# Performance work log

Hardware: AMD Instinct MI355X
Metric: run time of the kernel (lower is better)

The kernel has to match this reference:

```python
import jax, jax.numpy as jnp
import numpy as np

N, E, G = 50000, 400000, 2000
H, HEADS, HD = 128, 4, 32


def setup_inputs() -> dict:
    key = jax.random.key(0)
    ks = jax.random.split(key, 16)
    nrm = lambda k, shape, s=0.05: jax.random.normal(k, shape, dtype=jnp.float32) * s
    inp = {}
    inp["x"] = jax.random.normal(ks[0], (N, 39), dtype=jnp.float32)
    inp["edge_index"] = jax.random.randint(ks[1], (2, E), 0, N, dtype=jnp.int32)
    inp["edge_attr"] = jax.random.normal(ks[2], (E, 8), dtype=jnp.float32)
    inp["batch"] = jnp.sort(jax.random.randint(ks[3], (N,), 0, G, dtype=jnp.int32))
    inp["in_W"] = nrm(ks[4], (39, H)); inp["in_b"] = jnp.zeros((H,), jnp.float32)
    inp["in_g"] = jnp.ones((H,), jnp.float32); inp["in_beta"] = jnp.zeros((H,), jnp.float32)
    inp["Wl"] = nrm(ks[5], (3, H, H)); inp["Wr"] = nrm(ks[6], (3, H, H))
    inp["We"] = nrm(ks[7], (3, 8, H)); inp["att"] = nrm(ks[8], (3, HEADS, HD))
    inp["conv_b"] = jnp.zeros((3, H), jnp.float32)
    inp["bn_g"] = jnp.ones((3, H), jnp.float32); inp["bn_b"] = jnp.zeros((3, H), jnp.float32)
    inp["t1_W"] = nrm(ks[9], (3 * H, 256)); inp["t1_b"] = jnp.zeros((256,), jnp.float32)
    inp["t1_g"] = jnp.ones((256,), jnp.float32); inp["t1_beta"] = jnp.zeros((256,), jnp.float32)
    inp["t2_W"] = nrm(ks[10], (256, 128)); inp["t2_b"] = jnp.zeros((128,), jnp.float32)
    inp["t2_g"] = jnp.ones((128,), jnp.float32); inp["t2_beta"] = jnp.zeros((128,), jnp.float32)
    inp["head_W"] = nrm(ks[11], (128, 12)); inp["head_b"] = jnp.zeros((12,), jnp.float32)
    return inp


def _bn(h, g, b):
    # BatchNorm1d in training mode: normalize with batch statistics.
    m = h.mean(0)
    v = ((h - m) ** 2).mean(0)
    return g * (h - m) * jax.lax.rsqrt(v + 1e-5) + b


def reference(x, edge_index, edge_attr, batch, in_W, in_b, in_g, in_beta,
              Wl, Wr, We, att, conv_b, bn_g, bn_b,
              t1_W, t1_b, t1_g, t1_beta, t2_W, t2_b, t2_g, t2_beta,
              head_W, head_b):
    src, dst = edge_index[0], edge_index[1]  # messages flow src -> dst (PyG convention)
    xn = jax.nn.relu(_bn(x @ in_W + in_b, in_g, in_beta))  # [N, H]
    for l in range(3):  # three residual GATv2 layers
        xl = (xn @ Wl[l]).reshape(N, HEADS, HD)  # lin_l (source transform)
        xr = (xn @ Wr[l]).reshape(N, HEADS, HD)  # lin_r (target transform)
        ep = (edge_attr @ We[l]).reshape(E, HEADS, HD)
        m = jax.nn.leaky_relu(xl[src] + xr[dst] + ep, 0.2)  # [E, HEADS, HD]
        alpha = jnp.einsum('ehd,hd->eh', m, att[l])  # [E, HEADS]
        amax = jax.ops.segment_max(alpha, dst, num_segments=N)
        amax = jnp.where(jnp.isfinite(amax), amax, 0.0)  # nodes with no in-edges
        ae = jnp.exp(alpha - amax[dst])
        denom = jax.ops.segment_sum(ae, dst, num_segments=N)
        a = ae / (denom[dst] + 1e-16)  # scatter-softmax over neighborhoods
        agg = jax.ops.segment_sum(xl[src] * a[:, :, None], dst, num_segments=N)
        h = agg.reshape(N, H) + conv_b[l]
        h = jax.nn.elu(_bn(h, bn_g[l], bn_b[l]))
        xn = xn + h
    # 3-way global pooling per graph
    cnt = jax.ops.segment_sum(jnp.ones((N,), jnp.float32), batch, num_segments=G)
    sadd = jax.ops.segment_sum(xn, batch, num_segments=G)
    smean = sadd / jnp.maximum(cnt, 1.0)[:, None]
    smax = jax.ops.segment_max(xn, batch, num_segments=G)
    smax = jnp.where(cnt[:, None] > 0, smax, 0.0)
    xg = jnp.concatenate([smean, smax, sadd], axis=1)  # [G, 3H]
    t = jax.nn.relu(_bn(xg @ t1_W + t1_b, t1_g, t1_beta))
    t = jax.nn.relu(_bn(t @ t2_W + t2_b, t2_g, t2_beta))
    return jax.nn.sigmoid(t @ head_W + head_b)  # [G, 12]
```

## Files before the change

kernel.cpp:

```cpp
#include <hip/hip_runtime.h>
#include <math.h>


constexpr int N_ = 50000;
constexpr int E_ = 400000;
constexpr int G_ = 2000;
constexpr int H_ = 128;
constexpr int IN_ = 39;

__global__ __launch_bounds__(256) void hist_kernel(const int* __restrict__ keys, int n,
                                                   int* __restrict__ cnt) {
  for (int i = blockIdx.x * 256 + threadIdx.x; i < n; i += gridDim.x * 256)
    atomicAdd(&cnt[keys[i]], 1);
}

__global__ __launch_bounds__(1024) void scan_excl4(const int* __restrict__ in,
                                                   int* __restrict__ out, int n) {
  __shared__ int wsum[16];
  __shared__ int carry_s, chunk_tot;
  int t = threadIdx.x, lane = t & 63, wid = t >> 6;
  if (t == 0) carry_s = 0;
  __syncthreads();
  for (int base = 0; base < n; base += 4096) {
    int idx = base + t * 4;
    int4 v = make_int4(0, 0, 0, 0);
    if (idx + 3 < n) {
      v = *(const int4*)&in[idx];
    } else {
      if (idx < n) v.x = in[idx];
      if (idx + 1 < n) v.y = in[idx + 1];
      if (idx + 2 < n) v.z = in[idx + 2];
      if (idx + 3 < n) v.w = in[idx + 3];
    }
    int tsum = v.x + v.y + v.z + v.w;
    int x = tsum;
#pragma unroll
    for (int off = 1; off < 64; off <<= 1) {
      int y = __shfl_up(x, off, 64);
      if (lane >= off) x += y;
    }
    if (lane == 63) wsum[wid] = x;
    __syncthreads();
    if (t == 0) {
      int acc = 0;
#pragma unroll
      for (int w = 0; w < 16; w++) { int tmp = wsum[w]; wsum[w] = acc; acc += tmp; }
      chunk_tot = acc;
    }
    __syncthreads();
    int base_ex = carry_s + wsum[wid] + x - tsum;
    if (idx < n) out[idx] = base_ex;
    if (idx + 1 < n) out[idx + 1] = base_ex + v.x;
    if (idx + 2 < n) out[idx + 2] = base_ex + v.x + v.y;
    if (idx + 3 < n) out[idx + 3] = base_ex + v.x + v.y + v.z;
    __syncthreads();
    if (t == 0) carry_s += chunk_tot;
    __syncthreads();
  }
  if (t == 0) out[n] = carry_s;
}

__global__ __launch_bounds__(256) void goff_from_sorted(const int* __restrict__ batch,
                                                        int* __restrict__ goff) {
  int i = blockIdx.x * 256 + threadIdx.x;
  if (i >= N_) return;
  int bi = batch[i];
  int bp = (i == 0) ? -1 : batch[i - 1];
  for (int g = bp + 1; g <= bi; g++) goff[g] = i;
  if (i == N_ - 1) {
    for (int g = bi + 1; g <= G_; g++) goff[g] = N_;
  }
}

__global__ __launch_bounds__(256) void edge_scatter(const int* __restrict__ ei,
                                                    const float* __restrict__ ea,
                                                    int* __restrict__ cursor,
                                                    int* __restrict__ esrc,
                                                    float* __restrict__ eas) {
  int e = blockIdx.x * 256 + threadIdx.x;
  if (e >= E_) return;
  int src = ei[e];
  int dst = ei[E_ + e];
  int j = atomicAdd(&cursor[dst], 1);
  esrc[j] = src;
  const float4* eav = (const float4*)(ea + (size_t)e * 8);
  float4* dstp = (float4*)(eas + (size_t)j * 8);
  dstp[0] = eav[0];
  dstp[1] = eav[1];
}

__global__ __launch_bounds__(256) void in_gemm(const float* __restrict__ x,
                                               const float* __restrict__ W,
                                               const float* __restrict__ b,
                                               float* __restrict__ y,
                                               float* __restrict__ ssum,
                                               float* __restrict__ ssq) {
  __shared__ float xs[32][40];
  __shared__ float s1[256], s2[256];
  int t = threadIdx.x;
  int row0 = blockIdx.x * 32;
  for (int i = t; i < 32 * IN_; i += 256) {
    int r = i / IN_, k = i % IN_;
    int row = row0 + r;
    xs[r][k] = (row < N_) ? x[row * IN_ + k] : 0.f;
  }
  __syncthreads();
  int col = t & 127;
  int half = t >> 7;
  float acc[16];
#pragma unroll
  for (int r = 0; r < 16; r++) acc[r] = 0.f;
  for (int k = 0; k < IN_; k++) {
    float w = W[k * H_ + col];
#pragma unroll
    for (int r = 0; r < 16; r++) acc[r] = fmaf(xs[half * 16 + r][k], w, acc[r]);
  }
  float bb = b[col];
  float a1 = 0.f, a2 = 0.f;
#pragma unroll
  for (int r = 0; r < 16; r++) {
    int row = row0 + half * 16 + r;
    float v = acc[r] + bb;
    if (row < N_) {
      y[row * H_ + col] = v;
      a1 += v;
      a2 = fmaf(v, v, a2);
    }
  }
  s1[t] = a1; s2[t] = a2;
  __syncthreads();
  if (t < 128) {
    atomicAdd(&ssum[t], s1[t] + s1[t + 128]);
    atomicAdd(&ssq[t], s2[t] + s2[t + 128]);
  }
}

__global__ __launch_bounds__(256) void gemm_xlxr(const float* __restrict__ xn,
                                                 const float* __restrict__ Wlp,
                                                 const float* __restrict__ Wrp,
                                                 float* __restrict__ xl,
                                                 float* __restrict__ xr) {
  __shared__ float xs[64][16];
  __shared__ float wl_s[16][128];
  __shared__ float wr_s[16][128];
  int t = threadIdx.x;
  int tx = t & 31;
  int ty = t >> 5;
  int row0 = blockIdx.x * 64;
  float4 accl[8], accr[8];
#pragma unroll
  for (int r = 0; r < 8; r++) {
    accl[r] = make_float4(0.f, 0.f, 0.f, 0.f);
    accr[r] = make_float4(0.f, 0.f, 0.f, 0.f);
  }
  for (int kc = 0; kc < H_; kc += 16) {
    __syncthreads();
    {
      int r = t >> 2;
      int k4 = (t & 3) * 4;
      int row = row0 + r;
      float4 v = (row < N_) ? *(const float4*)&xn[row * H_ + kc + k4]
                            : make_float4(0.f, 0.f, 0.f, 0.f);
      *(float4*)&xs[r][k4] = v;
    }
    for (int i = t; i < 512; i += 256) {
      int k = i >> 5;
      int c4 = (i & 31) * 4;
      *(float4*)&wl_s[k][c4] = *(const float4*)&Wlp[(kc + k) * H_ + c4];
      *(float4*)&wr_s[k][c4] = *(const float4*)&Wrp[(kc + k) * H_ + c4];
    }
    __syncthreads();
#pragma unroll
    for (int k = 0; k < 16; k += 4) {
      float4 xv[8];
#pragma unroll
      for (int r = 0; r < 8; r++) xv[r] = *(const float4*)&xs[ty * 8 + r][k];
#pragma unroll
      for (int kk = 0; kk < 4; kk++) {
        float4 wl = *(const float4*)&wl_s[k + kk][tx * 4];
        float4 wr = *(const float4*)&wr_s[k + kk][tx * 4];
#pragma unroll
        for (int r = 0; r < 8; r++) {
          float xvr = (kk == 0) ? xv[r].x : (kk == 1) ? xv[r].y : (kk == 2) ? xv[r].z : xv[r].w;
          accl[r].x = fmaf(xvr, wl.x, accl[r].x);
          accl[r].y = fmaf(xvr, wl.y, accl[r].y);
          accl[r].z = fmaf(xvr, wl.z, accl[r].z);
          accl[r].w = fmaf(xvr, wl.w, accl[r].w);
          accr[r].x = fmaf(xvr, wr.x, accr[r].x);
          accr[r].y = fmaf(xvr, wr.y, accr[r].y);
          accr[r].z = fmaf(xvr, wr.z, accr[r].z);
          accr[r].w = fmaf(xvr, wr.w, accr[r].w);
        }
      }
    }
  }
#pragma unroll
  for (int r = 0; r < 8; r++) {
    int row = row0 + ty * 8 + r;
    if (row < N_) {
      *(float4*)&xl[row * H_ + tx * 4] = accl[r];
      *(float4*)&xr[row * H_ + tx * 4] = accr[r];
    }
  }
}

__device__ __forceinline__ float epcalc(const float4& a0, const float4& a1, const float w[8]) {
  float ep = a0.x * w[0];
  ep = fmaf(a0.y, w[1], ep);
  ep = fmaf(a0.z, w[2], ep);
  ep = fmaf(a0.w, w[3], ep);
  ep = fmaf(a1.x, w[4], ep);
  ep = fmaf(a1.y, w[5], ep);
  ep = fmaf(a1.z, w[6], ep);
  ep = fmaf(a1.w, w[7], ep);
  return ep;
}

__global__ __launch_bounds__(256) void agg_csr(const int* __restrict__ eoff,
                                               const int* __restrict__ esrc,
                                               const float* __restrict__ eas,
                                               const float* __restrict__ Wel,
                                               const float* __restrict__ attl,
                                               const float* __restrict__ xl,
                                               const float* __restrict__ xr,
                                               const float* __restrict__ cb,
                                               float* __restrict__ buf,
                                               float* __restrict__ ssum,
                                               float* __restrict__ ssq) {
  __shared__ float s1[256], s2[256];
  int t = threadIdx.x;
  int lane = t & 127;
  int sub = t >> 7;
  float w[8];
#pragma unroll
  for (int k = 0; k < 8; k++) w[k] = Wel[k * H_ + lane];
  float attv = attl[lane];
  float cbv = cb[lane];
  float a1 = 0.f, a2 = 0.f;
  for (int n = blockIdx.x * 2 + sub; n < N_; n += gridDim.x * 2) {
    float xrv = xr[n * H_ + lane];
    int e0 = eoff[n], e1 = eoff[n + 1];
    float acc = 0.f, den = 0.f;
    int j = e0;
    for (; j + 4 <= e1; j += 4) {
      int s0 = esrc[j], s1i = esrc[j + 1], s2i = esrc[j + 2], s3 = esrc[j + 3];
      const float4* ep0 = (const float4*)(eas + (size_t)j * 8);
      float4 a00 = ep0[0], a01 = ep0[1];
      float4 a10 = ep0[2], a11 = ep0[3];
      float4 a20 = ep0[4], a21 = ep0[5];
      float4 a30 = ep0[6], a31 = ep0[7];
      float x0 = xl[s0 * H_ + lane];
      float x1 = xl[s1i * H_ + lane];
      float x2 = xl[s2i * H_ + lane];
      float x3 = xl[s3 * H_ + lane];
      float m0 = x0 + xrv + epcalc(a00, a01, w);
      float m1 = x1 + xrv + epcalc(a10, a11, w);
      float m2 = x2 + xrv + epcalc(a20, a21, w);
      float m3 = x3 + xrv + epcalc(a30, a31, w);
      m0 = (m0 > 0.f) ? m0 : 0.2f * m0;
      m1 = (m1 > 0.f) ? m1 : 0.2f * m1;
      m2 = (m2 > 0.f) ? m2 : 0.2f * m2;
      m3 = (m3 > 0.f) ? m3 : 0.2f * m3;
      float p0 = m0 * attv, p1 = m1 * attv, p2 = m2 * attv, p3 = m3 * attv;
#pragma unroll
      for (int off = 16; off > 0; off >>= 1) {
        p0 += __shfl_xor(p0, off, 64);
        p1 += __shfl_xor(p1, off, 64);
        p2 += __shfl_xor(p2, off, 64);
        p3 += __shfl_xor(p3, off, 64);
      }
      float e0v = __expf(p0), e1v = __expf(p1), e2v = __expf(p2), e3v = __expf(p3);
      acc = fmaf(e0v, x0, acc);
      acc = fmaf(e1v, x1, acc);
      acc = fmaf(e2v, x2, acc);
      acc = fmaf(e3v, x3, acc);
      den += (e0v + e1v) + (e2v + e3v);
    }
    for (; j < e1; j++) {
      int src = esrc[j];
      const float4* eap = (const float4*)(eas + (size_t)j * 8);
      float4 ea0 = eap[0], ea1 = eap[1];
      float xlv = xl[src * H_ + lane];
      float m = xlv + xrv + epcalc(ea0, ea1, w);
      m = (m > 0.f) ? m : 0.2f * m;
      float p = m * attv;
#pragma unroll
      for (int off = 16; off > 0; off >>= 1) p += __shfl_xor(p, off, 64);
      float ae = __expf(p);
      acc = fmaf(ae, xlv, acc);
      den += ae;
    }
    float h = acc / (den + 1e-16f) + cbv;
    buf[n * H_ + lane] = h;
    a1 += h;
    a2 = fmaf(h, h, a2);
  }
  s1[t] = a1; s2[t] = a2;
  __syncthreads();
  if (t < 128) {
    atomicAdd(&ssum[t], s1[t] + s1[t + 128]);
    atomicAdd(&ssq[t], s2[t] + s2[t + 128]);
  }
}

__global__ void bn_final(const float* __restrict__ ssum, const float* __restrict__ ssq,
                         float rows_inv, int cols, float* __restrict__ mean,
                         float* __restrict__ rstd) {
  int c = threadIdx.x;
  if (c < cols) {
    float m = ssum[c] * rows_inv;
    float v = ssq[c] * rows_inv - m * m;
    mean[c] = m;
    rstd[c] = rsqrtf(v + 1e-5f);
  }
}

__global__ __launch_bounds__(256) void apply_bn_relu(const float* __restrict__ y,
                                                     float* __restrict__ out,
                                                     const float* __restrict__ g,
                                                     const float* __restrict__ beta,
                                                     const float* __restrict__ mean,
                                                     const float* __restrict__ rstd,
                                                     long total, int cmask) {
  long i = (long)blockIdx.x * 256 + threadIdx.x;
  if (i >= total) return;
  int c = (int)i & cmask;
  float v = g[c] * (y[i] - mean[c]) * rstd[c] + beta[c];
  out[i] = fmaxf(v, 0.f);
}

__global__ __launch_bounds__(256) void node_residual(float* __restrict__ xn,
                                                     const float* __restrict__ buf,
                                                     const float* __restrict__ g,
                                                     const float* __restrict__ beta,
                                                     const float* __restrict__ mean,
                                                     const float* __restrict__ rstd) {
  int i = blockIdx.x * 256 + threadIdx.x;
  if (i >= N_ * H_) return;
  int c = i & 127;
  float v = g[c] * (buf[i] - mean[c]) * rstd[c] + beta[c];
  v = (v > 0.f) ? v : (__expf(v) - 1.f);
  xn[i] += v;
}

__global__ __launch_bounds__(128) void pool_csr(const int* __restrict__ goff,
                                                const float* __restrict__ xn,
                                                float* __restrict__ xg) {
  int g = blockIdx.x;
  int t = threadIdx.x;
  int n0 = goff[g], n1 = goff[g + 1];
  float s = 0.f, mx = -INFINITY;
  for (int n = n0; n < n1; n++) {
    float v = xn[n * H_ + t];
    s += v;
    mx = fmaxf(mx, v);
  }
  float c = (float)(n1 - n0);
  xg[g * 384 + t] = s / fmaxf(c, 1.f);
  xg[g * 384 + 128 + t] = (c > 0.f) ? mx : 0.f;
  xg[g * 384 + 256 + t] = s;
}

template <int K, int COLS>
__global__ void mlp_gemm(const float* __restrict__ A, const float* __restrict__ W,
                         const float* __restrict__ b, float* __restrict__ Y, int rows,
                         float* __restrict__ ssum, float* __restrict__ ssq) {
  __shared__ float xs[8][K];
  int t = threadIdx.x;
  int row0 = blockIdx.x * 8;
  for (int i = t; i < 8 * K; i += COLS) {
    int r = i / K, k = i % K;
    int row = row0 + r;
    xs[r][k] = (row < rows) ? A[row * K + k] : 0.f;
  }
  __syncthreads();
  float acc[8];
#pragma unroll
  for (int r = 0; r < 8; r++) acc[r] = 0.f;
  for (int k = 0; k < K; k++) {
    float w = W[k * COLS + t];
#pragma unroll
    for (int r = 0; r < 8; r++) acc[r] = fmaf(xs[r][k], w, acc[r]);
  }
  float bb = b[t];
  float a1 = 0.f, a2 = 0.f;
#pragma unroll
  for (int r = 0; r < 8; r++) {
    int row = row0 + r;
    if (row < rows) {
      float v = acc[r] + bb;
      Y[row * COLS + t] = v;
      a1 += v;
      a2 = fmaf(v, v, a2);
    }
  }
  atomicAdd(&ssum[t], a1);
  atomicAdd(&ssq[t], a2);
}

__global__ __launch_bounds__(64) void head_kernel(const float* __restrict__ u,
                                                  const float* __restrict__ W,
                                                  const float* __restrict__ b,
                                                  float* __restrict__ out) {
  __shared__ float row[128];
  int g = blockIdx.x;
  int t = threadIdx.x;
  row[t] = u[g * 128 + t];
  row[t + 64] = u[g * 128 + 64 + t];
  __syncthreads();
  if (t < 12) {
    float acc = b[t];
    for (int k = 0; k < 128; k++) acc = fmaf(row[k], W[k * 12 + t], acc);
    out[g * 12 + t] = 1.f / (1.f + expf(-acc));
  }
}

extern "C" void kernel_launch(void* const* d_in, const int* in_sizes, int n_in, void* d_out,
                              int out_size, void* d_ws, size_t ws_size, hipStream_t stream) {
  (void)in_sizes; (void)n_in; (void)out_size; (void)ws_size;
  const float* x       = (const float*)d_in[0];
  const int*   ei      = (const int*)d_in[1];
  const float* ea      = (const float*)d_in[2];
  const int*   batch   = (const int*)d_in[3];
  const float* in_W    = (const float*)d_in[4];
  const float* in_b    = (const float*)d_in[5];
  const float* in_g    = (const float*)d_in[6];
  const float* in_beta = (const float*)d_in[7];
  const float* Wl      = (const float*)d_in[8];
  const float* Wr      = (const float*)d_in[9];
  const float* We      = (const float*)d_in[10];
  const float* att     = (const float*)d_in[11];
  const float* conv_b  = (const float*)d_in[12];
  const float* bn_g    = (const float*)d_in[13];
  const float* bn_b    = (const float*)d_in[14];
  const float* t1_W    = (const float*)d_in[15];
  const float* t1_b    = (const float*)d_in[16];
  const float* t1_g    = (const float*)d_in[17];
  const float* t1_beta = (const float*)d_in[18];
  const float* t2_W    = (const float*)d_in[19];
  const float* t2_b    = (const float*)d_in[20];
  const float* t2_g    = (const float*)d_in[21];
  const float* t2_beta = (const float*)d_in[22];
  const float* head_W  = (const float*)d_in[23];
  const float* head_b  = (const float*)d_in[24];
  float* out = (float*)d_out;

  float* p = (float*)d_ws;
  float* xn   = p; p += N_ * H_;
  float* xl   = p; p += N_ * H_;
  float* xr   = p; p += N_ * H_;
  float* buf  = p; p += N_ * H_;
  float* ssum = p; p += 256;
  float* ssq  = p; p += 256;
  float* mean = p; p += 256;
  float* rstd = p; p += 256;
  float* xg   = p; p += G_ * 384;
  float* u1   = p; p += G_ * 256;
  float* u2   = p; p += G_ * 128;
  float* eas  = p; p += (size_t)E_ * 8;
  int* ip = (int*)p;
  int* deg    = ip; ip += N_;
  int* eoff   = ip; ip += N_ + 1;
  int* cursor = ip; ip += N_;
  int* goff   = ip; ip += G_ + 1;
  int* esrc   = ip; ip += E_;

  const int EW_GRID = 25000;

  hipMemsetAsync(deg, 0, (size_t)N_ * sizeof(int), stream);
  hist_kernel<<<1024, 256, 0, stream>>>(ei + E_, E_, deg);
  scan_excl4<<<1, 1024, 0, stream>>>(deg, eoff, N_);
  hipMemcpyAsync(cursor, eoff, (size_t)N_ * sizeof(int), hipMemcpyDeviceToDevice, stream);
  edge_scatter<<<(E_ + 255) / 256, 256, 0, stream>>>(ei, ea, cursor, esrc, eas);
  goff_from_sorted<<<(N_ + 255) / 256, 256, 0, stream>>>(batch, goff);

  hipMemsetAsync(ssum, 0, 512 * sizeof(float), stream);
  in_gemm<<<(N_ + 31) / 32, 256, 0, stream>>>(x, in_W, in_b, buf, ssum, ssq);
  bn_final<<<1, 256, 0, stream>>>(ssum, ssq, 1.f / N_, H_, mean, rstd);
  apply_bn_relu<<<EW_GRID, 256, 0, stream>>>(buf, xn, in_g, in_beta, mean, rstd,
                                             (long)N_ * H_, 127);

  for (int l = 0; l < 3; l++) {
    gemm_xlxr<<<(N_ + 63) / 64, 256, 0, stream>>>(xn, Wl + l * H_ * H_, Wr + l * H_ * H_, xl, xr);
    hipMemsetAsync(ssum, 0, 512 * sizeof(float), stream);
    agg_csr<<<4096, 256, 0, stream>>>(eoff, esrc, eas, We + l * 8 * H_, att + l * H_,
                                      xl, xr, conv_b + l * H_, buf, ssum, ssq);
    bn_final<<<1, 256, 0, stream>>>(ssum, ssq, 1.f / N_, H_, mean, rstd);
    node_residual<<<EW_GRID, 256, 0, stream>>>(xn, buf, bn_g + l * H_, bn_b + l * H_, mean, rstd);
  }

  pool_csr<<<G_, 128, 0, stream>>>(goff, xn, xg);

  hipMemsetAsync(ssum, 0, 512 * sizeof(float), stream);
  mlp_gemm<384, 256><<<G_ / 8, 256, 0, stream>>>(xg, t1_W, t1_b, u1, G_, ssum, ssq);
  bn_final<<<1, 256, 0, stream>>>(ssum, ssq, 1.f / G_, 256, mean, rstd);
  apply_bn_relu<<<(G_ * 256 + 255) / 256, 256, 0, stream>>>(u1, u1, t1_g, t1_beta, mean, rstd,
                                                            (long)G_ * 256, 255);

  hipMemsetAsync(ssum, 0, 512 * sizeof(float), stream);
  mlp_gemm<256, 128><<<G_ / 8, 128, 0, stream>>>(u1, t2_W, t2_b, u2, G_, ssum, ssq);
  bn_final<<<1, 256, 0, stream>>>(ssum, ssq, 1.f / G_, 128, mean, rstd);
  apply_bn_relu<<<(G_ * 128 + 255) / 256, 256, 0, stream>>>(u2, u2, t2_g, t2_beta, mean, rstd,
                                                            (long)G_ * 128, 127);

  head_kernel<<<G_, 64, 0, stream>>>(u2, head_W, head_b, out);
}
```

Baseline: 963.7 us.

## Fuse BN/activation/residual into GEMM prologue and widen aggregation to float2 lanes

The BN+ReLU after the input layer and the BN+ELU+residual after each GATv2 layer now run inside the load stage of the following xl/xr GEMM, which also writes the updated xn back. This removes separate elementwise passes over the N×H arrays. The aggregation kernel now gives each lane two channels (64 lanes per node, 4 nodes per block), so each warp handles wider float2 gathers with shorter shuffle reductions. bn_final zeroes its accumulators, and the scan writes the cursor copy directly, which drops several memsets and a device memcpy. The cost is some redundant BN math in every GEMM tile and more register pressure in agg_csr.

```diff
diff --git a/kernel.cpp b/kernel.cpp
--- a/kernel.cpp
+++ b/kernel.cpp
@@ -15,7 +15,8 @@
 }
 
 __global__ __launch_bounds__(1024) void scan_excl4(const int* __restrict__ in,
-                                                   int* __restrict__ out, int n) {
+                                                   int* __restrict__ out,
+                                                   int* __restrict__ out2, int n) {
   __shared__ int wsum[16];
   __shared__ int carry_s, chunk_tot;
   int t = threadIdx.x, lane = t & 63, wid = t >> 6;
@@ -48,11 +49,11 @@
       chunk_tot = acc;
     }
     __syncthreads();
-    int base_ex = carry_s + wsum[wid] + x - tsum;
-    if (idx < n) out[idx] = base_ex;
-    if (idx + 1 < n) out[idx + 1] = base_ex + v.x;
-    if (idx + 2 < n) out[idx + 2] = base_ex + v.x + v.y;
-    if (idx + 3 < n) out[idx + 3] = base_ex + v.x + v.y + v.z;
+    int b0 = carry_s + wsum[wid] + x - tsum;
+    if (idx < n) { out[idx] = b0; out2[idx] = b0; }
+    if (idx + 1 < n) { out[idx + 1] = b0 + v.x; out2[idx + 1] = b0 + v.x; }
+    if (idx + 2 < n) { out[idx + 2] = b0 + v.x + v.y; out2[idx + 2] = b0 + v.x + v.y; }
+    if (idx + 3 < n) { out[idx + 3] = b0 + v.x + v.y + v.z; out2[idx + 3] = b0 + v.x + v.y + v.z; }
     __syncthreads();
     if (t == 0) carry_s += chunk_tot;
     __syncthreads();
@@ -135,7 +136,14 @@
   }
 }
 
-__global__ __launch_bounds__(256) void gemm_xlxr(const float* __restrict__ xn,
+template <int MODE>
+__global__ __launch_bounds__(256) void gemm_xlxr(const float* __restrict__ xn_ro,
+                                                 float* __restrict__ xn,
+                                                 const float* __restrict__ buf,
+                                                 const float* __restrict__ g,
+                                                 const float* __restrict__ beta,
+                                                 const float* __restrict__ mean,
+                                                 const float* __restrict__ rstd,
                                                  const float* __restrict__ Wlp,
                                                  const float* __restrict__ Wrp,
                                                  float* __restrict__ xl,
@@ -159,8 +167,33 @@
       int r = t >> 2;
       int k4 = (t & 3) * 4;
       int row = row0 + r;
-      float4 v = (row < N_) ? *(const float4*)&xn[row * H_ + kc + k4]
-                            : make_float4(0.f, 0.f, 0.f, 0.f);
+      int c = kc + k4;
+      float4 v = make_float4(0.f, 0.f, 0.f, 0.f);
+      if (row < N_) {
+        if (MODE == 0) {
+          v = *(const float4*)&xn_ro[row * H_ + c];
+        } else {
+          float4 bv = *(const float4*)&buf[row * H_ + c];
+          float4 gv = *(const float4*)&g[c];
+          float4 be = *(const float4*)&beta[c];
+          float4 mn = *(const float4*)&mean[c];
+          float4 rs = *(const float4*)&rstd[c];
+          float t0 = gv.x * (bv.x - mn.x) * rs.x + be.x;
+          float t1 = gv.y * (bv.y - mn.y) * rs.y + be.y;
+          float t2 = gv.z * (bv.z - mn.z) * rs.z + be.z;
+          float t3 = gv.w * (bv.w - mn.w) * rs.w + be.w;
+          if (MODE == 1) {
+            v = make_float4(fmaxf(t0, 0.f), fmaxf(t1, 0.f), fmaxf(t2, 0.f), fmaxf(t3, 0.f));
+          } else {
+            float4 xo = *(const float4*)&xn[row * H_ + c];
+            v.x = xo.x + ((t0 > 0.f) ? t0 : (__expf(t0) - 1.f));
+            v.y = xo.y + ((t1 > 0.f) ? t1 : (__expf(t1) - 1.f));
+            v.z = xo.z + ((t2 > 0.f) ? t2 : (__expf(t2) - 1.f));
+            v.w = xo.w + ((t3 > 0.f) ? t3 : (__expf(t3) - 1.f));
+          }
+          *(float4*)&xn[row * H_ + c] = v;
+        }
+      }
       *(float4*)&xs[r][k4] = v;
     }
     for (int i = t; i < 512; i += 256) {
@@ -204,7 +237,7 @@
   }
 }
 
-__device__ __forceinline__ float epcalc(const float4& a0, const float4& a1, const float w[8]) {
+__device__ __forceinline__ float ep8(const float4& a0, const float4& a1, const float* w) {
   float ep = a0.x * w[0];
   ep = fmaf(a0.y, w[1], ep);
   ep = fmaf(a0.z, w[2], ep);
@@ -227,91 +260,119 @@
                                                float* __restrict__ buf,
                                                float* __restrict__ ssum,
                                                float* __restrict__ ssq) {
-  __shared__ float s1[256], s2[256];
+  __shared__ float sA[256], sB[256], sC[256], sD[256];
   int t = threadIdx.x;
-  int lane = t & 127;
-  int sub = t >> 7;
-  float w[8];
-#pragma unroll
-  for (int k = 0; k < 8; k++) w[k] = Wel[k * H_ + lane];
-  float attv = attl[lane];
-  float cbv = cb[lane];
-  float a1 = 0.f, a2 = 0.f;
-  for (int n = blockIdx.x * 2 + sub; n < N_; n += gridDim.x * 2) {
-    float xrv = xr[n * H_ + lane];
+  int l = t & 63;
+  int sub = t >> 6;
+  int c0 = l * 2;
+  float w0[8], w1[8];
+#pragma unroll
+  for (int k = 0; k < 8; k++) {
+    float2 wv = *(const float2*)&Wel[k * H_ + c0];
+    w0[k] = wv.x; w1[k] = wv.y;
+  }
+  float2 attv = *(const float2*)&attl[c0];
+  float2 cbv = *(const float2*)&cb[c0];
+  const float2* xl2 = (const float2*)xl;
+  float a1_0 = 0.f, a1_1 = 0.f, a2_0 = 0.f, a2_1 = 0.f;
+  for (int n = blockIdx.x * 4 + sub; n < N_; n += gridDim.x * 4) {
+    float2 xrv = *(const float2*)&xr[n * H_ + c0];
     int e0 = eoff[n], e1 = eoff[n + 1];
-    float acc = 0.f, den = 0.f;
+    float acc0 = 0.f, acc1 = 0.f, den = 0.f;
     int j = e0;
     for (; j + 4 <= e1; j += 4) {
-      int s0 = esrc[j], s1i = esrc[j + 1], s2i = esrc[j + 2], s3 = esrc[j + 3];
-      const float4* ep0 = (const float4*)(eas + (size_t)j * 8);
-      float4 a00 = ep0[0], a01 = ep0[1];
-      float4 a10 = ep0[2], a11 = ep0[3];
-      float4 a20 = ep0[4], a21 = ep0[5];
-      float4 a30 = ep0[6], a31 = ep0[7];
-      float x0 = xl[s0 * H_ + lane];
-      float x1 = xl[s1i * H_ + lane];
-      float x2 = xl[s2i * H_ + lane];
-      float x3 = xl[s3 * H_ + lane];
-      float m0 = x0 + xrv + epcalc(a00, a01, w);
-      float m1 = x1 + xrv + epcalc(a10, a11, w);
-      float m2 = x2 + xrv + epcalc(a20, a21, w);
-      float m3 = x3 + xrv + epcalc(a30, a31, w);
-      m0 = (m0 > 0.f) ? m0 : 0.2f * m0;
-      m1 = (m1 > 0.f) ? m1 : 0.2f * m1;
-      m2 = (m2 > 0.f) ? m2 : 0.2f * m2;
-      m3 = (m3 > 0.f) ? m3 : 0.2f * m3;
-      float p0 = m0 * attv, p1 = m1 * attv, p2 = m2 * attv, p3 = m3 * attv;
-#pragma unroll
-      for (int off = 16; off > 0; off >>= 1) {
+      int s0 = esrc[j], s1 = esrc[j + 1], s2 = esrc[j + 2], s3 = esrc[j + 3];
+      const float4* ep = (const float4*)(eas + (size_t)j * 8);
+      float4 a00 = ep[0], a01 = ep[1];
+      float4 a10 = ep[2], a11 = ep[3];
+      float4 a20 = ep[4], a21 = ep[5];
+      float4 a30 = ep[6], a31 = ep[7];
+      float2 x0 = xl2[(size_t)s0 * 64 + l];
+      float2 x1 = xl2[(size_t)s1 * 64 + l];
+      float2 x2 = xl2[(size_t)s2 * 64 + l];
+      float2 x3 = xl2[(size_t)s3 * 64 + l];
+      float m00 = x0.x + xrv.x + ep8(a00, a01, w0);
+      float m01 = x0.y + xrv.y + ep8(a00, a01, w1);
+      float m10 = x1.x + xrv.x + ep8(a10, a11, w0);
+      float m11 = x1.y + xrv.y + ep8(a10, a11, w1);
+      float m20 = x2.x + xrv.x + ep8(a20, a21, w0);
+      float m21 = x2.y + xrv.y + ep8(a20, a21, w1);
+      float m30 = x3.x + xrv.x + ep8(a30, a31, w0);
+      float m31 = x3.y + xrv.y + ep8(a30, a31, w1);
+      m00 = (m00 > 0.f) ? m00 : 0.2f * m00;
+      m01 = (m01 > 0.f) ? m01 : 0.2f * m01;
+      m10 = (m10 > 0.f) ? m10 : 0.2f * m10;
+      m11 = (m11 > 0.f) ? m11 : 0.2f * m11;
+      m20 = (m20 > 0.f) ? m20 : 0.2f * m20;
+      m21 = (m21 > 0.f) ? m21 : 0.2f * m21;
+      m30 = (m30 > 0.f) ? m30 : 0.2f * m30;
+      m31 = (m31 > 0.f) ? m31 : 0.2f * m31;
+      float p0 = fmaf(m00, attv.x, m01 * attv.y);
+      float p1 = fmaf(m10, attv.x, m11 * attv.y);
+      float p2 = fmaf(m20, attv.x, m21 * attv.y);
+      float p3 = fmaf(m30, attv.x, m31 * attv.y);
+#pragma unroll
+      for (int off = 8; off > 0; off >>= 1) {
         p0 += __shfl_xor(p0, off, 64);
         p1 += __shfl_xor(p1, off, 64);
         p2 += __shfl_xor(p2, off, 64);
         p3 += __shfl_xor(p3, off, 64);
       }
       float e0v = __expf(p0), e1v = __expf(p1), e2v = __expf(p2), e3v = __expf(p3);
-      acc = fmaf(e0v, x0, acc);
-      acc = fmaf(e1v, x1, acc);
-      acc = fmaf(e2v, x2, acc);
-      acc = fmaf(e3v, x3, acc);
+      acc0 = fmaf(e0v, x0.x, acc0); acc1 = fmaf(e0v, x0.y, acc1);
+      acc0 = fmaf(e1v, x1.x, acc0); acc1 = fmaf(e1v, x1.y, acc1);
+      acc0 = fmaf(e2v, x2.x, acc0); acc1 = fmaf(e2v, x2.y, acc1);
+      acc0 = fmaf(e3v, x3.x, acc0); acc1 = fmaf(e3v, x3.y, acc1);
       den += (e0v + e1v) + (e2v + e3v);
     }
     for (; j < e1; j++) {
-      int src = esrc[j];
-      const float4* eap = (const float4*)(eas + (size_t)j * 8);
-      float4 ea0 = eap[0], ea1 = eap[1];
-      float xlv = xl[src * H_ + lane];
-      float m = xlv + xrv + epcalc(ea0, ea1, w);
-      m = (m > 0.f) ? m : 0.2f * m;
-      float p = m * attv;
-#pragma unroll
-      for (int off = 16; off > 0; off >>= 1) p += __shfl_xor(p, off, 64);
-      float ae = __expf(p);
-      acc = fmaf(ae, xlv, acc);
-      den += ae;
-    }
-    float h = acc / (den + 1e-16f) + cbv;
-    buf[n * H_ + lane] = h;
-    a1 += h;
-    a2 = fmaf(h, h, a2);
-  }
-  s1[t] = a1; s2[t] = a2;
+      int s0 = esrc[j];
+      const float4* ep = (const float4*)(eas + (size_t)j * 8);
+      float4 a00 = ep[0], a01 = ep[1];
+      float2 x0 = xl2[(size_t)s0 * 64 + l];
+      float m00 = x0.x + xrv.x + ep8(a00, a01, w0);
+      float m01 = x0.y + xrv.y + ep8(a00, a01, w1);
+      m00 = (m00 > 0.f) ? m00 : 0.2f * m00;
+      m01 = (m01 > 0.f) ? m01 : 0.2f * m01;
+      float p0 = fmaf(m00, attv.x, m01 * attv.y);
+#pragma unroll
+      for (int off = 8; off > 0; off >>= 1) p0 += __shfl_xor(p0, off, 64);
+      float e0v = __expf(p0);
+      acc0 = fmaf(e0v, x0.x, acc0);
+      acc1 = fmaf(e0v, x0.y, acc1);
+      den += e0v;
+    }
+    float inv = 1.f / (den + 1e-16f);
+    float h0 = acc0 * inv + cbv.x;
+    float h1 = acc1 * inv + cbv.y;
+    *(float2*)&buf[n * H_ + c0] = make_float2(h0, h1);
+    a1_0 += h0; a1_1 += h1;
+    a2_0 = fmaf(h0, h0, a2_0); a2_1 = fmaf(h1, h1, a2_1);
+  }
+  sA[t] = a1_0; sB[t] = a1_1; sC[t] = a2_0; sD[t] = a2_1;
   __syncthreads();
-  if (t < 128) {
-    atomicAdd(&ssum[t], s1[t] + s1[t + 128]);
-    atomicAdd(&ssq[t], s2[t] + s2[t + 128]);
-  }
-}
-
-__global__ void bn_final(const float* __restrict__ ssum, const float* __restrict__ ssq,
-                         float rows_inv, int cols, float* __restrict__ mean,
-                         float* __restrict__ rstd) {
+  if (t < 64) {
+    float r1 = sA[t] + sA[t + 64] + sA[t + 128] + sA[t + 192];
+    float r2 = sB[t] + sB[t + 64] + sB[t + 128] + sB[t + 192];
+    float r3 = sC[t] + sC[t + 64] + sC[t + 128] + sC[t + 192];
+    float r4 = sD[t] + sD[t + 64] + sD[t + 128] + sD[t + 192];
+    atomicAdd(&ssum[2 * t], r1);
+    atomicAdd(&ssum[2 * t + 1], r2);
+    atomicAdd(&ssq[2 * t], r3);
+    atomicAdd(&ssq[2 * t + 1], r4);
+  }
+}
+
+__global__ void bn_final(float* __restrict__ ssum, float* __restrict__ ssq, float rows_inv,
+                         int cols, float* __restrict__ mean, float* __restrict__ rstd) {
   int c = threadIdx.x;
   if (c < cols) {
     float m = ssum[c] * rows_inv;
     float v = ssq[c] * rows_inv - m * m;
     mean[c] = m;
     rstd[c] = rsqrtf(v + 1e-5f);
+    ssum[c] = 0.f;
+    ssq[c] = 0.f;
   }
 }
 
@@ -465,39 +526,37 @@
   int* goff   = ip; ip += G_ + 1;
   int* esrc   = ip; ip += E_;
 
-  const int EW_GRID = 25000;
-
   hipMemsetAsync(deg, 0, (size_t)N_ * sizeof(int), stream);
   hist_kernel<<<1024, 256, 0, stream>>>(ei + E_, E_, deg);
-  scan_excl4<<<1, 1024, 0, stream>>>(deg, eoff, N_);
-  hipMemcpyAsync(cursor, eoff, (size_t)N_ * sizeof(int), hipMemcpyDeviceToDevice, stream);
+  scan_excl4<<<1, 1024, 0, stream>>>(deg, eoff, cursor, N_);
   edge_scatter<<<(E_ + 255) / 256, 256, 0, stream>>>(ei, ea, cursor, esrc, eas);
   goff_from_sorted<<<(N_ + 255) / 256, 256, 0, stream>>>(batch, goff);
 
   hipMemsetAsync(ssum, 0, 512 * sizeof(float), stream);
   in_gemm<<<(N_ + 31) / 32, 256, 0, stream>>>(x, in_W, in_b, buf, ssum, ssq);
   bn_final<<<1, 256, 0, stream>>>(ssum, ssq, 1.f / N_, H_, mean, rstd);
-  apply_bn_relu<<<EW_GRID, 256, 0, stream>>>(buf, xn, in_g, in_beta, mean, rstd,
-                                             (long)N_ * H_, 127);
 
   for (int l = 0; l < 3; l++) {
-    gemm_xlxr<<<(N_ + 63) / 64, 256, 0, stream>>>(xn, Wl + l * H_ * H_, Wr + l * H_ * H_, xl, xr);
-    hipMemsetAsync(ssum, 0, 512 * sizeof(float), stream);
-    agg_csr<<<4096, 256, 0, stream>>>(eoff, esrc, eas, We + l * 8 * H_, att + l * H_,
+    if (l == 0) {
+      gemm_xlxr<1><<<(N_ + 63) / 64, 256, 0, stream>>>(xn, xn, buf, in_g, in_beta, mean, rstd,
+                                                       Wl + l * H_ * H_, Wr + l * H_ * H_, xl, xr);
+    } else {
+      gemm_xlxr<2><<<(N_ + 63) / 64, 256, 0, stream>>>(xn, xn, buf, bn_g + (l - 1) * H_,
+                                                       bn_b + (l - 1) * H_, mean, rstd,
+                                                       Wl + l * H_ * H_, Wr + l * H_ * H_, xl, xr);
+    }
+    agg_csr<<<2048, 256, 0, stream>>>(eoff, esrc, eas, We + l * 8 * H_, att + l * H_,
                                       xl, xr, conv_b + l * H_, buf, ssum, ssq);
     bn_final<<<1, 256, 0, stream>>>(ssum, ssq, 1.f / N_, H_, mean, rstd);
-    node_residual<<<EW_GRID, 256, 0, stream>>>(xn, buf, bn_g + l * H_, bn_b + l * H_, mean, rstd);
-  }
-
+  }
+  node_residual<<<25000, 256, 0, stream>>>(xn, buf, bn_g + 2 * H_, bn_b + 2 * H_, mean, rstd);
   pool_csr<<<G_, 128, 0, stream>>>(goff, xn, xg);
 
-  hipMemsetAsync(ssum, 0, 512 * sizeof(float), stream);
   mlp_gemm<384, 256><<<G_ / 8, 256, 0, stream>>>(xg, t1_W, t1_b, u1, G_, ssum, ssq);
   bn_final<<<1, 256, 0, stream>>>(ssum, ssq, 1.f / G_, 256, mean, rstd);
   apply_bn_relu<<<(G_ * 256 + 255) / 256, 256, 0, stream>>>(u1, u1, t1_g, t1_beta, mean, rstd,
                                                             (long)G_ * 256, 255);
 
-  hipMemsetAsync(ssum, 0, 512 * sizeof(float), stream);
   mlp_gemm<256, 128><<<G_ / 8, 128, 0, stream>>>(u1, t2_W, t2_b, u2, G_, ssum, ssq);
   bn_final<<<1, 256, 0, stream>>>(ssum, ssq, 1.f / G_, 128, mean, rstd);
   apply_bn_relu<<<(G_ * 128 + 255) / 256, 256, 0, stream>>>(u2, u2, t2_g, t2_beta, mean, rstd,
```

Measured after the change: 911.7 us. -5.4%, faster.
